# Performance work log

Measured on AMD Instinct MI355X. Metric: run time of the kernel, lower is better.

The kernel has to match this reference:

```python
import jax, jax.numpy as jnp
import numpy as np

EPS = 1e-5
GROUPS = 4


def gconv1x1(x, w, b, groups):
    # x: [B,C,H,W]; w: [Cout, Cin//groups]; grouped 1x1 conv
    B, C, H, W = x.shape
    Co = w.shape[0]
    xg = x.reshape(B, groups, C // groups, H, W)
    wg = w.reshape(groups, Co // groups, C // groups)
    y = jnp.einsum('bgchw,goc->bgohw', xg, wg).reshape(B, Co, H, W)
    if b is not None:
        y = y + b[None, :, None, None]
    return y


def setup_inputs() -> dict:
    key = jax.random.key(0)
    ks = jax.random.split(key, 9)
    B, C, H, W = 8, 64, 160, 160
    Cq = C // 8
    s = 0.1
    return {
        'x': jax.random.normal(ks[0], (B, C, H, W), jnp.float32),
        'wq': jax.random.normal(ks[1], (Cq, C // GROUPS), jnp.float32) * s,
        'bq': jax.random.normal(ks[2], (Cq,), jnp.float32) * s,
        'wk': jax.random.normal(ks[3], (Cq, C // GROUPS), jnp.float32) * s,
        'bk': jax.random.normal(ks[4], (Cq,), jnp.float32) * s,
        'wv': jax.random.normal(ks[5], (C, C // GROUPS), jnp.float32) * s,
        'bv': jax.random.normal(ks[6], (C,), jnp.float32) * s,
        'gamma': jax.random.normal(ks[7], (1,), jnp.float32) * s,
        'w1d': jax.random.normal(ks[8], (C, C // GROUPS), jnp.float32) * s,
        'bn_w': jnp.ones((C,), jnp.float32),
        'bn_b': jnp.zeros((C,), jnp.float32),
    }


def reference(x, wq, bq, wk, bk, wv, bv, gamma, w1d, bn_w, bn_b):
    B, C, H, W = x.shape
    q = gconv1x1(x, wq, bq, GROUPS)   # [B,Cq,H,W]
    k = gconv1x1(x, wk, bk, GROUPS)   # [B,Cq,H,W]
    v = gconv1x1(x, wv, bv, GROUPS)   # [B,C,H,W]

    # column (H) attention energies with -inf diagonal (self excluded on H path)
    energy_H = jnp.einsum('bchw,bcjw->bhwj', q, k)  # [B,H,W,H]
    diag = jnp.where(jnp.eye(H, dtype=bool), -jnp.inf, 0.0).astype(x.dtype)
    energy_H = energy_H + diag[:, None, :]
    # row (W) attention energies
    energy_W = jnp.einsum('bchw,bchj->bhwj', q, k)  # [B,H,W,W]

    att = jax.nn.softmax(jnp.concatenate([energy_H, energy_W], axis=3), axis=3)
    att_H = att[..., :H]           # [B,H,W,H]
    att_W = att[..., H:]           # [B,H,W,W]

    out_H = jnp.einsum('bcjw,bhwj->bchw', v, att_H)
    out_W = jnp.einsum('bchj,bhwj->bchw', v, att_W)
    out = gamma[0] * (out_H + out_W)               # [B,C,H,W]

    # kernel-size-1 grouped conv1d (dilation irrelevant for k=1), no bias
    L = H * W
    o = out.reshape(B, GROUPS, C // GROUPS, L)
    w1g = w1d.reshape(GROUPS, C // GROUPS, C // GROUPS)
    o = jnp.einsum('bgcl,goc->bgol', o, w1g).reshape(B, C, L)

    # BatchNorm1d (training mode: batch stats over (B, L), biased variance)
    mean = jnp.mean(o, axis=(0, 2), keepdims=True)
    var = jnp.mean((o - mean) ** 2, axis=(0, 2), keepdims=True)
    o = (o - mean) / jnp.sqrt(var + EPS) * bn_w[None, :, None] + bn_b[None, :, None]

    o = o.reshape(B, C, H, W)
    return jax.nn.relu(o + x)
```

## Files before the change

### kernel.cpp

```cpp
#include <hip/hip_runtime.h>
#include <math.h>

#define B_ 8
#define C_ 64
#define H_ 160
#define W_ 160
#define HW_ (H_*W_)

typedef _Float16 h2 __attribute__((ext_vector_type(2)));
typedef _Float16 h4 __attribute__((ext_vector_type(4)));
typedef _Float16 h8 __attribute__((ext_vector_type(8)));
typedef float f4v __attribute__((ext_vector_type(4)));
union H8u { h8 v; h2 h[4]; };

__device__ inline float fdot2(h2 a, h2 b, float c) {
    return __builtin_amdgcn_fdot2(a, b, c, false);
}

#define LOG2E 1.44269504088896f
#define ESH2  5.77078016355585f
#if __has_builtin(__builtin_amdgcn_exp2f)
#define EXP2F(x) __builtin_amdgcn_exp2f(x)
#else
#define EXP2F(x) exp2f(x)
#endif

static constexpr size_t N_PIX  = (size_t)B_*H_*W_;
static constexpr size_t N_FULL = (size_t)B_*H_*W_*C_;
static constexpr size_t OFF_OUTH  = 0;
static constexpr size_t OFF_VROW  = N_FULL/2;
static constexpr size_t OFF_QROW  = OFF_VROW + N_FULL/2;
static constexpr size_t OFF_KROW  = OFF_QROW + N_PIX*4;
static constexpr size_t OFF_MH    = OFF_KROW + N_PIX*4;
static constexpr size_t OFF_SH    = OFF_MH + N_PIX;
static constexpr size_t OFF_BNSUM = OFF_SH + N_PIX;
static constexpr size_t OFF_BNSQ  = OFF_BNSUM + 64;

__global__ __launch_bounds__(256,4) void qkv_kernel(
    const float* __restrict__ x,
    const float* __restrict__ wq, const float* __restrict__ bq,
    const float* __restrict__ wk, const float* __restrict__ bk,
    const float* __restrict__ wv, const float* __restrict__ bv,
    _Float16* __restrict__ qrow, _Float16* __restrict__ krow,
    _Float16* __restrict__ vrow)
{
    __shared__ __align__(16) _Float16 spool[10240];
    _Float16 (*xsh)[72] = (_Float16 (*)[72])spool;

    const int tid = threadIdx.x;
    const int w0 = blockIdx.x * 32;
    const int h0 = blockIdx.y * 4;
    const int b  = blockIdx.z;

    const float* xb = x + (size_t)b*C_*HW_;
    for (int i = tid; i < 2048; i += 256) {
        int w4 = i & 7;
        int c  = ((i >> 3) & 7) | (((i >> 6) & 7) << 3);
        int hh = i >> 9;
        float4 v = *(const float4*)(xb + (size_t)c*HW_ + (size_t)(h0+hh)*W_ + w0 + w4*4);
        int pix = hh*32 + w4*4;
        xsh[pix+0][c] = (_Float16)v.x; xsh[pix+1][c] = (_Float16)v.y;
        xsh[pix+2][c] = (_Float16)v.z; xsh[pix+3][c] = (_Float16)v.w;
    }
    __syncthreads();

    const int lane = tid & 63;
    const int wid  = tid >> 6;
    const int n16  = lane & 15;
    const int kg   = lane >> 4;
    const int pb   = wid * 32;

    h4 af[2][4];
    #pragma unroll
    for (int sub = 0; sub < 2; sub++)
        #pragma unroll
        for (int g = 0; g < 4; g++)
            af[sub][g] = *(const h4*)&xsh[pb + sub*16 + n16][g*16 + 4*kg];

    f4v vacc[2][4];
    #pragma unroll
    for (int g = 0; g < 4; g++) {
        float4 wf = *(const float4*)(wv + (g*16 + n16)*16 + 4*kg);
        h4 bf; bf[0]=(_Float16)wf.x; bf[1]=(_Float16)wf.y;
               bf[2]=(_Float16)wf.z; bf[3]=(_Float16)wf.w;
        const float bb = bv[g*16 + n16];
        #pragma unroll
        for (int sub = 0; sub < 2; sub++) {
            f4v c = {bb, bb, bb, bb};
            vacc[sub][g] = __builtin_amdgcn_mfma_f32_16x16x16f16(af[sub][g], bf, c, 0, 0, 0);
        }
    }
    f4v qkacc[2];
    {
        const int out = n16;
        const int gq  = (out & 7) >> 1;
        const float sc = (out < 8) ? LOG2E : 1.0f;
        const float* wp = ((out < 8) ? wq + out*16 : wk + (out-8)*16) + 4*kg;
        float4 wf = *(const float4*)wp;
        h4 bfq; bfq[0]=(_Float16)(wf.x*sc); bfq[1]=(_Float16)(wf.y*sc);
                bfq[2]=(_Float16)(wf.z*sc); bfq[3]=(_Float16)(wf.w*sc);
        h4 bz;  bz[0]=(_Float16)0; bz[1]=(_Float16)0; bz[2]=(_Float16)0; bz[3]=(_Float16)0;
        const float bb = ((out < 8) ? bq[out] : bk[out-8]) * sc;
        #pragma unroll
        for (int sub = 0; sub < 2; sub++) {
            f4v c = {bb, bb, bb, bb};
            #pragma unroll
            for (int g = 0; g < 4; g++) {
                h4 bg = (gq == g) ? bfq : bz;
                c = __builtin_amdgcn_mfma_f32_16x16x16f16(af[sub][g], bg, c, 0, 0, 0);
            }
            qkacc[sub] = c;
        }
    }
    __syncthreads();

    _Float16* vst = spool;
    _Float16* qks = spool + 8192;
    #pragma unroll
    for (int sub = 0; sub < 2; sub++) {
        #pragma unroll
        for (int r = 0; r < 4; r++) {
            int pix = pb + sub*16 + 4*kg + r;
            #pragma unroll
            for (int g = 0; g < 4; g++)
                vst[pix*64 + g*16 + n16] = (_Float16)vacc[sub][g][r];
            qks[pix*16 + n16] = (_Float16)qkacc[sub][r];
        }
    }
    __syncthreads();

    unsigned* vs32 = (unsigned*)spool;
    unsigned* qk32 = vs32 + 4096;
    unsigned* vrow32 = (unsigned*)vrow;
    for (int i = tid; i < 4096; i += 256) {
        int pix = i >> 5, cp = i & 31;
        size_t bp = ((size_t)b*H_ + h0 + (pix>>5))*W_ + w0 + (pix & 31);
        vrow32[bp*32 + cp] = vs32[i];
    }
    unsigned* qrow32 = (unsigned*)qrow;
    unsigned* krow32 = (unsigned*)krow;
    for (int i = tid; i < 1024; i += 256) {
        int pix = i >> 3, part = i & 7;
        size_t bp = ((size_t)b*H_ + h0 + (pix>>5))*W_ + w0 + (pix & 31);
        unsigned val = qk32[pix*8 + part];
        if (part < 4) qrow32[bp*4 + part]     = val;
        else          krow32[bp*4 + part - 4] = val;
    }
}

__global__ __launch_bounds__(256,4) void passA_kernel(
    const _Float16* __restrict__ qrow, const _Float16* __restrict__ krow,
    const _Float16* __restrict__ vrow,
    _Float16* __restrict__ outH, float* __restrict__ sH)
{
    __shared__ __align__(16) _Float16 pool[10240];
    __shared__ __align__(16) _Float16 q2h[160][8];
    __shared__ __align__(16) _Float16 k2h[160][8];
    __shared__ float psum2[2][2][32];

    _Float16* v2s = pool;

    const int tid = threadIdx.x;
    const int b = blockIdx.x / W_;
    const int w = blockIdx.x % W_;

    if (tid < 160) {
        size_t bp = ((size_t)b*H_ + tid)*W_ + w;
        *(int4*)&q2h[tid][0] = *(const int4*)(qrow + bp*8);
        *(int4*)&k2h[tid][0] = *(const int4*)(krow + bp*8);
    }
    {
        const unsigned* vr32 = (const unsigned*)vrow;
        const int cp = tid & 31, hp0 = tid >> 5;
        #pragma unroll 5
        for (int it = 0; it < 10; it++) {
            int hp = hp0 + 8*it;
            int kt = hp >> 4, dqv = (hp >> 2) & 3, jj = 2*(hp & 3);
            size_t bp0 = ((size_t)b*H_ + 2*hp)*W_ + w;
            unsigned u0 = vr32[bp0*32 + cp];
            unsigned u1 = vr32[(bp0 + W_)*32 + cp];
            unsigned e  = __builtin_amdgcn_perm(u1, u0, 0x05040100);
            unsigned o  = __builtin_amdgcn_perm(u1, u0, 0x07060302);
            int base = ((kt*4 + dqv)*64 + 2*cp)*8 + jj;
            *(unsigned*)&v2s[base]     = e;
            *(unsigned*)&v2s[base + 8] = o;
        }
    }
    __syncthreads();

    const int lane = tid & 63;
    const int wid  = tid >> 6;
    const int cM   = wid*16 + (lane & 15);
    const int m_   = lane & 15;
    const int dq   = lane >> 4;
    const int n16  = lane & 15;
    const int kg   = lane >> 4;
    const int qs   = wid & 1;
    const int jt0  = (wid >> 1)*5;

    h8 vfr[5];
    #pragma unroll
    for (int kt = 0; kt < 5; kt++)
        vfr[kt] = *(const h8*)&v2s[((kt*4 + dq)*64 + cM)*8];
    __syncthreads();

    for (int t = 0; t <= 5; t++) {
        if (t <= 4) {
            _Float16* Pts = pool + (t & 1)*5120;
            const int q32  = qs*16 + n16;
            const int qrw  = t*32 + q32;
            h4 qf = *(const h4*)&q2h[qrw][(kg & 1)*4];
            if (kg >= 2) { qf[0]=(_Float16)0; qf[1]=(_Float16)0; qf[2]=(_Float16)0; qf[3]=(_Float16)0; }
            float psloc = 0.f;
            #pragma unroll
            for (int jj = 0; jj < 5; jj++) {
                const int jt = jt0 + jj;
                h4 kf = *(const h4*)&k2h[jt*16 + n16][(kg & 1)*4];
                f4v d = {0.f,0.f,0.f,0.f};
                d = __builtin_amdgcn_mfma_f32_16x16x16f16(kf, qf, d, 0, 0, 0);
                const int grp = (jt >> 1)*4 + (jt & 1)*2 + (kg >> 1);
                h4 pk;
                #pragma unroll
                for (int r = 0; r < 4; r++) {
                    float p = EXP2F(d[r] - ESH2);
                    if (jt*16 + kg*4 + r == qrw) p = 0.f;
                    psloc += p;
                    pk[r] = (_Float16)p;
                }
                *(h4*)&Pts[(grp*32 + q32)*8 + (kg & 1)*4] = pk;
            }
            psloc += __shfl_xor(psloc, 16);
            psloc += __shfl_xor(psloc, 32);
            if (kg == 0) psum2[t & 1][wid >> 1][q32] = psloc;
        }
        if (t >= 1) {
            if (tid < 32) {
                sH[((size_t)b*W_ + w)*H_ + (t-1)*32 + tid] =
                    psum2[(t-1) & 1][0][tid] + psum2[(t-1) & 1][1][tid];
            }
            const _Float16* Pts = pool + ((t-1) & 1)*5120;
            f4v acc0 = {0.f,0.f,0.f,0.f}, acc1 = {0.f,0.f,0.f,0.f};
            #pragma unroll
            for (int kt = 0; kt < 5; kt++) {
                h8 a0  = *(const h8*)&Pts[((kt*4 + dq)*32 + m_)*8];
                h8 a1  = *(const h8*)&Pts[((kt*4 + dq)*32 + 16 + m_)*8];
                acc0 = __builtin_amdgcn_mfma_f32_16x16x32_f16(a0, vfr[kt], acc0, 0, 0, 0);
                acc1 = __builtin_amdgcn_mfma_f32_16x16x32_f16(a1, vfr[kt], acc1, 0, 0, 0);
            }
            #pragma unroll
            for (int r = 0; r < 4; r++) {
                int r0 = (t-1)*32 + dq*4 + r;
                outH[(((size_t)b*H_ + r0     )*W_ + w)*64 + cM] = (_Float16)acc0[r];
                outH[(((size_t)b*H_ + r0 + 16)*W_ + w)*64 + cM] = (_Float16)acc1[r];
            }
        }
        if (t <= 4) __syncthreads();
    }
}

__global__ __launch_bounds__(256,4) void passB_kernel(
    const _Float16* __restrict__ qrow, const _Float16* __restrict__ krow,
    const _Float16* vrow,
    const float* __restrict__ gamma, const float* __restrict__ w1d,
    const _Float16* __restrict__ outH, const float* __restrict__ sH,
    _Float16* o16, float* __restrict__ bnsum, float* __restrict__ bnsq)
{
    __shared__ __align__(16) _Float16 pool[10240];
    __shared__ __align__(16) _Float16 stageh[4*32*20];
    __shared__ __align__(16) _Float16 q2h[160][8];
    __shared__ __align__(16) _Float16 k2h[160][8];
    __shared__ float sHrow[160];
    __shared__ float psum2[2][2][32];

    _Float16* v2s = pool;

    const int tid = threadIdx.x;
    const int b = blockIdx.x / H_;
    const int h = blockIdx.x % H_;
    const float gam = gamma[0];

    const int lane = tid & 63;
    const int wid  = tid >> 6;
    const int cM   = wid*16 + (lane & 15);
    const int m_   = lane & 15;
    const int dq   = lane >> 4;
    const int n16  = lane & 15;
    const int kg   = lane >> 4;
    const int qs   = wid & 1;
    const int jt0  = (wid >> 1)*5;

    h4 w1f;
    {
        float4 wv4 = *(const float4*)(w1d + cM*16 + 4*dq);
        w1f[0] = (_Float16)wv4.x; w1f[1] = (_Float16)wv4.y;
        w1f[2] = (_Float16)wv4.z; w1f[3] = (_Float16)wv4.w;
    }

    const size_t rowbase = ((size_t)b*H_ + h)*W_;
    if (tid < 160) {
        size_t bp = rowbase + tid;
        *(int4*)&q2h[tid][0] = *(const int4*)(qrow + bp*8);
        *(int4*)&k2h[tid][0] = *(const int4*)(krow + bp*8);
        sHrow[tid] = sH[((size_t)b*W_ + tid)*H_ + h];
    }
    {
        const unsigned* vr32 = (const unsigned*)vrow;
        const int cp = tid & 31, wp0 = tid >> 5;
        #pragma unroll 5
        for (int it = 0; it < 10; it++) {
            int wp = wp0 + 8*it;
            int kt = wp >> 4, dqv = (wp >> 2) & 3, jj = 2*(wp & 3);
            size_t bp0 = rowbase + 2*wp;
            unsigned u0 = vr32[bp0*32 + cp];
            unsigned u1 = vr32[(bp0 + 1)*32 + cp];
            unsigned e  = __builtin_amdgcn_perm(u1, u0, 0x05040100);
            unsigned o  = __builtin_amdgcn_perm(u1, u0, 0x07060302);
            int base = ((kt*4 + dqv)*64 + 2*cp)*8 + jj;
            *(unsigned*)&v2s[base]     = e;
            *(unsigned*)&v2s[base + 8] = o;
        }
    }
    __syncthreads();

    h8 vfr[5];
    #pragma unroll
    for (int kt = 0; kt < 5; kt++)
        vfr[kt] = *(const h8*)&v2s[((kt*4 + dq)*64 + cM)*8];
    __syncthreads();

    float bnS = 0.f, bnS2 = 0.f;

    for (int t = 0; t <= 5; t++) {
        float oh0[4], oh1[4];
        if (t >= 1) {
            #pragma unroll
            for (int r = 0; r < 4; r++) {
                int rw0 = (t-1)*32 + dq*4 + r;
                oh0[r] = (float)outH[(rowbase + rw0     )*64 + cM];
                oh1[r] = (float)outH[(rowbase + rw0 + 16)*64 + cM];
            }
        }
        if (t <= 4) {
            _Float16* Pts = pool + (t & 1)*5120;
            const int q32 = qs*16 + n16;
            const int qrw = t*32 + q32;
            h4 qf = *(const h4*)&q2h[qrw][(kg & 1)*4];
            if (kg >= 2) { qf[0]=(_Float16)0; qf[1]=(_Float16)0; qf[2]=(_Float16)0; qf[3]=(_Float16)0; }
            float psloc = 0.f;
            #pragma unroll
            for (int jj = 0; jj < 5; jj++) {
                const int jt = jt0 + jj;
                h4 kf = *(const h4*)&k2h[jt*16 + n16][(kg & 1)*4];
                f4v d = {0.f,0.f,0.f,0.f};
                d = __builtin_amdgcn_mfma_f32_16x16x16f16(kf, qf, d, 0, 0, 0);
                const int grp = (jt >> 1)*4 + (jt & 1)*2 + (kg >> 1);
                h4 pk;
                #pragma unroll
                for (int r = 0; r < 4; r++) {
                    float p = EXP2F(d[r] - ESH2);
                    psloc += p;
                    pk[r] = (_Float16)p;
                }
                *(h4*)&Pts[(grp*32 + q32)*8 + (kg & 1)*4] = pk;
            }
            psloc += __shfl_xor(psloc, 16);
            psloc += __shfl_xor(psloc, 32);
            if (kg == 0) psum2[t & 1][wid >> 1][q32] = psloc;
        }
        if (t >= 1) {
            const int tp = t - 1;
            const _Float16* Pts = pool + (tp & 1)*5120;
            const int rl_ = lane & 31;
            float fval = gam / (sHrow[tp*32 + rl_]
                                + psum2[tp & 1][0][rl_] + psum2[tp & 1][1][rl_]);
            f4v acc0 = {0.f,0.f,0.f,0.f}, acc1 = {0.f,0.f,0.f,0.f};
            #pragma unroll
            for (int kt = 0; kt < 5; kt++) {
                h8 a0  = *(const h8*)&Pts[((kt*4 + dq)*32 + m_)*8];
                h8 a1  = *(const h8*)&Pts[((kt*4 + dq)*32 + 16 + m_)*8];
                acc0 = __builtin_amdgcn_mfma_f32_16x16x32_f16(a0, vfr[kt], acc0, 0, 0, 0);
                acc1 = __builtin_amdgcn_mfma_f32_16x16x32_f16(a1, vfr[kt], acc1, 0, 0, 0);
            }
            _Float16* st = &stageh[wid*640];
            #pragma unroll
            for (int r = 0; r < 4; r++) {
                int rl0 = dq*4 + r, rl1 = rl0 + 16;
                float f0 = __shfl(fval, rl0);
                float f1 = __shfl(fval, rl1);
                st[rl0*20 + m_] = (_Float16)((oh0[r] + acc0[r]) * f0);
                st[rl1*20 + m_] = (_Float16)((oh1[r] + acc1[r]) * f1);
            }
            h4 a0c = *(const h4*)&st[m_*20 + 4*dq];
            h4 a1c = *(const h4*)&st[(m_ + 16)*20 + 4*dq];
            f4v c0 = {0.f,0.f,0.f,0.f}, c1 = {0.f,0.f,0.f,0.f};
            c0 = __builtin_amdgcn_mfma_f32_16x16x16f16(a0c, w1f, c0, 0, 0, 0);
            c1 = __builtin_amdgcn_mfma_f32_16x16x16f16(a1c, w1f, c1, 0, 0, 0);
            #pragma unroll
            for (int r = 0; r < 4; r++) {
                int pr0 = dq*4 + r, pr1 = pr0 + 16;
                float o0 = c0[r], o1 = c1[r];
                o16[(rowbase + tp*32 + pr0)*64 + cM] = (_Float16)o0;
                o16[(rowbase + tp*32 + pr1)*64 + cM] = (_Float16)o1;
                bnS  += o0 + o1;
                bnS2 += o0*o0 + o1*o1;
            }
        }
        if (t <= 4) __syncthreads();
    }
    bnS  += __shfl_xor(bnS, 16);  bnS  += __shfl_xor(bnS, 32);
    bnS2 += __shfl_xor(bnS2, 16); bnS2 += __shfl_xor(bnS2, 32);
    if (dq == 0) {
        atomicAdd(&bnsum[cM], bnS);
        atomicAdd(&bnsq[cM],  bnS2);
    }
}

__global__ __launch_bounds__(256) void final_kernel(
    const float* __restrict__ x, const _Float16* __restrict__ o16,
    const float* __restrict__ bnsum, const float* __restrict__ bnsq,
    const float* __restrict__ bn_w, const float* __restrict__ bn_b,
    float* __restrict__ out)
{
    __shared__ _Float16 olds[160*66];
    __shared__ float sc[64], sh[64];
    const int tid = threadIdx.x;
    const int b = blockIdx.x / H_, h = blockIdx.x % H_;
    if (tid < 64) {
        const float cnt = (float)(B_*H_*W_);
        float mean = bnsum[tid] / cnt;
        float var  = bnsq[tid] / cnt - mean*mean;
        float istd = rsqrtf(var + 1e-5f);
        float scl  = bn_w[tid] * istd;
        sc[tid] = scl;
        sh[tid] = bn_b[tid] - mean*scl;
    }
    const unsigned* op = (const unsigned*)(o16 + ((size_t)b*H_ + h)*W_*64);
    unsigned* ol32 = (unsigned*)olds;
    for (int i = tid; i < 5120; i += 256) {
        int w = i >> 5, c2 = i & 31;
        ol32[w*33 + c2] = op[i];
    }
    __syncthreads();
    const float* xr = x   + (size_t)b*C_*HW_ + (size_t)h*W_;
    float*       ob = out + (size_t)b*C_*HW_ + (size_t)h*W_;
    for (int i = tid; i < 64*160; i += 256) {
        int c = i / 160, w = i - c*160;
        float v = (float)olds[w*66 + c] * sc[c] + sh[c] + xr[(size_t)c*HW_ + w];
        ob[(size_t)c*HW_ + w] = fmaxf(v, 0.f);
    }
}

extern "C" void kernel_launch(void* const* d_in, const int* in_sizes, int n_in,
                              void* d_out, int out_size, void* d_ws, size_t ws_size,
                              hipStream_t stream)
{
    (void)in_sizes; (void)n_in; (void)out_size; (void)ws_size;
    const float* x     = (const float*)d_in[0];
    const float* wq    = (const float*)d_in[1];
    const float* bq    = (const float*)d_in[2];
    const float* wk    = (const float*)d_in[3];
    const float* bk    = (const float*)d_in[4];
    const float* wv    = (const float*)d_in[5];
    const float* bv    = (const float*)d_in[6];
    const float* gamma = (const float*)d_in[7];
    const float* w1d   = (const float*)d_in[8];
    const float* bn_w  = (const float*)d_in[9];
    const float* bn_b  = (const float*)d_in[10];

    float* ws = (float*)d_ws;
    _Float16* outH16 = (_Float16*)(ws + OFF_OUTH);
    _Float16* vrow   = (_Float16*)(ws + OFF_VROW);
    _Float16* qrow   = (_Float16*)(ws + OFF_QROW);
    _Float16* krow   = (_Float16*)(ws + OFF_KROW);
    float* sH    = ws + OFF_SH;
    float* bnsum = ws + OFF_BNSUM;
    float* bnsq  = ws + OFF_BNSQ;
    _Float16* o16 = vrow;

    (void)hipMemsetAsync(bnsum, 0, 128*sizeof(float), stream);

    dim3 qgrid(W_/32, H_/4, B_);
    qkv_kernel<<<qgrid, 256, 0, stream>>>(x, wq, bq, wk, bk, wv, bv, qrow, krow, vrow);
    passA_kernel<<<B_*W_, 256, 0, stream>>>(qrow, krow, vrow, outH16, sH);
    passB_kernel<<<B_*H_, 256, 0, stream>>>(qrow, krow, vrow, gamma, w1d,
                                            outH16, sH, o16, bnsum, bnsq);
    final_kernel<<<B_*H_, 256, 0, stream>>>(x, o16, bnsum, bnsq, bn_w, bn_b, (float*)d_out);
}
```

Measured before the change: 206.7 us.

## Split attention passes across query tiles into separate blocks, write output in place

Pass A and pass B now launch five blocks per column or row, one per 32-query tile, where before one block looped over all five tiles with double-buffered P. This adds parallelism and drops the per-tile loop and its barriers. In exchange, each block reloads the full V column or row and the K vectors, so V staging traffic goes up fivefold. Pass B also writes its conv output back into the outH buffer in place instead of a separate o16 buffer, and BN atomics now fire once per block, five times as often.

```diff
diff --git a/kernel.cpp b/kernel.cpp
--- a/kernel.cpp
+++ b/kernel.cpp
@@ -154,20 +154,27 @@
     _Float16* __restrict__ outH, float* __restrict__ sH)
 {
     __shared__ __align__(16) _Float16 pool[10240];
-    __shared__ __align__(16) _Float16 q2h[160][8];
+    __shared__ __align__(16) _Float16 q2h[32][8];
     __shared__ __align__(16) _Float16 k2h[160][8];
-    __shared__ float psum2[2][2][32];
+    __shared__ float psum2[2][32];
 
     _Float16* v2s = pool;
+    _Float16* Pts = pool;
 
     const int tid = threadIdx.x;
-    const int b = blockIdx.x / W_;
-    const int w = blockIdx.x % W_;
+    const int bx  = blockIdx.x;
+    const int t   = bx % 5;
+    const int col = bx / 5;
+    const int b = col / W_;
+    const int w = col % W_;
 
     if (tid < 160) {
         size_t bp = ((size_t)b*H_ + tid)*W_ + w;
-        *(int4*)&q2h[tid][0] = *(const int4*)(qrow + bp*8);
         *(int4*)&k2h[tid][0] = *(const int4*)(krow + bp*8);
+        if (tid < 32) {
+            size_t bq = ((size_t)b*H_ + t*32 + tid)*W_ + w;
+            *(int4*)&q2h[tid][0] = *(const int4*)(qrow + bq*8);
+        }
     }
     {
         const unsigned* vr32 = (const unsigned*)vrow;
@@ -204,79 +211,78 @@
         vfr[kt] = *(const h8*)&v2s[((kt*4 + dq)*64 + cM)*8];
     __syncthreads();
 
-    for (int t = 0; t <= 5; t++) {
-        if (t <= 4) {
-            _Float16* Pts = pool + (t & 1)*5120;
-            const int q32  = qs*16 + n16;
-            const int qrw  = t*32 + q32;
-            h4 qf = *(const h4*)&q2h[qrw][(kg & 1)*4];
-            if (kg >= 2) { qf[0]=(_Float16)0; qf[1]=(_Float16)0; qf[2]=(_Float16)0; qf[3]=(_Float16)0; }
-            float psloc = 0.f;
-            #pragma unroll
-            for (int jj = 0; jj < 5; jj++) {
-                const int jt = jt0 + jj;
-                h4 kf = *(const h4*)&k2h[jt*16 + n16][(kg & 1)*4];
-                f4v d = {0.f,0.f,0.f,0.f};
-                d = __builtin_amdgcn_mfma_f32_16x16x16f16(kf, qf, d, 0, 0, 0);
-                const int grp = (jt >> 1)*4 + (jt & 1)*2 + (kg >> 1);
-                h4 pk;
-                #pragma unroll
-                for (int r = 0; r < 4; r++) {
-                    float p = EXP2F(d[r] - ESH2);
-                    if (jt*16 + kg*4 + r == qrw) p = 0.f;
-                    psloc += p;
-                    pk[r] = (_Float16)p;
-                }
-                *(h4*)&Pts[(grp*32 + q32)*8 + (kg & 1)*4] = pk;
-            }
-            psloc += __shfl_xor(psloc, 16);
-            psloc += __shfl_xor(psloc, 32);
-            if (kg == 0) psum2[t & 1][wid >> 1][q32] = psloc;
-        }
-        if (t >= 1) {
-            if (tid < 32) {
-                sH[((size_t)b*W_ + w)*H_ + (t-1)*32 + tid] =
-                    psum2[(t-1) & 1][0][tid] + psum2[(t-1) & 1][1][tid];
-            }
-            const _Float16* Pts = pool + ((t-1) & 1)*5120;
-            f4v acc0 = {0.f,0.f,0.f,0.f}, acc1 = {0.f,0.f,0.f,0.f};
-            #pragma unroll
-            for (int kt = 0; kt < 5; kt++) {
-                h8 a0  = *(const h8*)&Pts[((kt*4 + dq)*32 + m_)*8];
-                h8 a1  = *(const h8*)&Pts[((kt*4 + dq)*32 + 16 + m_)*8];
-                acc0 = __builtin_amdgcn_mfma_f32_16x16x32_f16(a0, vfr[kt], acc0, 0, 0, 0);
-                acc1 = __builtin_amdgcn_mfma_f32_16x16x32_f16(a1, vfr[kt], acc1, 0, 0, 0);
-            }
+    {
+        const int q32  = qs*16 + n16;
+        const int qrw  = t*32 + q32;
+        h4 qf = *(const h4*)&q2h[q32][(kg & 1)*4];
+        if (kg >= 2) { qf[0]=(_Float16)0; qf[1]=(_Float16)0; qf[2]=(_Float16)0; qf[3]=(_Float16)0; }
+        float psloc = 0.f;
+        #pragma unroll
+        for (int jj = 0; jj < 5; jj++) {
+            const int jt = jt0 + jj;
+            h4 kf = *(const h4*)&k2h[jt*16 + n16][(kg & 1)*4];
+            f4v d = {0.f,0.f,0.f,0.f};
+            d = __builtin_amdgcn_mfma_f32_16x16x16f16(kf, qf, d, 0, 0, 0);
+            const int grp = (jt >> 1)*4 + (jt & 1)*2 + (kg >> 1);
+            h4 pk;
             #pragma unroll
             for (int r = 0; r < 4; r++) {
-                int r0 = (t-1)*32 + dq*4 + r;
-                outH[(((size_t)b*H_ + r0     )*W_ + w)*64 + cM] = (_Float16)acc0[r];
-                outH[(((size_t)b*H_ + r0 + 16)*W_ + w)*64 + cM] = (_Float16)acc1[r];
+                float p = EXP2F(d[r] - ESH2);
+                if (jt*16 + kg*4 + r == qrw) p = 0.f;
+                psloc += p;
+                pk[r] = (_Float16)p;
             }
-        }
-        if (t <= 4) __syncthreads();
+            *(h4*)&Pts[(grp*32 + q32)*8 + (kg & 1)*4] = pk;
+        }
+        psloc += __shfl_xor(psloc, 16);
+        psloc += __shfl_xor(psloc, 32);
+        if (kg == 0) psum2[wid >> 1][q32] = psloc;
+    }
+    __syncthreads();
+
+    if (tid < 32)
+        sH[((size_t)b*W_ + w)*H_ + t*32 + tid] = psum2[0][tid] + psum2[1][tid];
+
+    f4v acc0 = {0.f,0.f,0.f,0.f}, acc1 = {0.f,0.f,0.f,0.f};
+    #pragma unroll
+    for (int kt = 0; kt < 5; kt++) {
+        h8 a0  = *(const h8*)&Pts[((kt*4 + dq)*32 + m_)*8];
+        h8 a1  = *(const h8*)&Pts[((kt*4 + dq)*32 + 16 + m_)*8];
+        acc0 = __builtin_amdgcn_mfma_f32_16x16x32_f16(a0, vfr[kt], acc0, 0, 0, 0);
+        acc1 = __builtin_amdgcn_mfma_f32_16x16x32_f16(a1, vfr[kt], acc1, 0, 0, 0);
+    }
+    #pragma unroll
+    for (int r = 0; r < 4; r++) {
+        int r0 = t*32 + dq*4 + r;
+        outH[(((size_t)b*H_ + r0     )*W_ + w)*64 + cM] = (_Float16)acc0[r];
+        outH[(((size_t)b*H_ + r0 + 16)*W_ + w)*64 + cM] = (_Float16)acc1[r];
     }
 }
 
 __global__ __launch_bounds__(256,4) void passB_kernel(
     const _Float16* __restrict__ qrow, const _Float16* __restrict__ krow,
-    const _Float16* vrow,
+    const _Float16* __restrict__ vrow,
     const float* __restrict__ gamma, const float* __restrict__ w1d,
-    const _Float16* __restrict__ outH, const float* __restrict__ sH,
-    _Float16* o16, float* __restrict__ bnsum, float* __restrict__ bnsq)
+    _Float16* outHio,
+    const float* __restrict__ sH,
+    float* __restrict__ bnsum, float* __restrict__ bnsq)
 {
     __shared__ __align__(16) _Float16 pool[10240];
-    __shared__ __align__(16) _Float16 stageh[4*32*20];
-    __shared__ __align__(16) _Float16 q2h[160][8];
+    __shared__ __align__(16) _Float16 q2h[32][8];
     __shared__ __align__(16) _Float16 k2h[160][8];
-    __shared__ float sHrow[160];
-    __shared__ float psum2[2][2][32];
+    __shared__ float sHrow[32];
+    __shared__ float psum2[2][32];
 
     _Float16* v2s = pool;
+    _Float16* Pts = pool;
+    _Float16* stageh = pool + 5120;
 
     const int tid = threadIdx.x;
-    const int b = blockIdx.x / H_;
-    const int h = blockIdx.x % H_;
+    const int bx  = blockIdx.x;
+    const int t   = bx % 5;
+    const int row = bx / 5;
+    const int b = row / H_;
+    const int h = row % H_;
     const float gam = gamma[0];
 
     const int lane = tid & 63;
@@ -299,9 +305,12 @@
     const size_t rowbase = ((size_t)b*H_ + h)*W_;
     if (tid < 160) {
         size_t bp = rowbase + tid;
-        *(int4*)&q2h[tid][0] = *(const int4*)(qrow + bp*8);
         *(int4*)&k2h[tid][0] = *(const int4*)(krow + bp*8);
-        sHrow[tid] = sH[((size_t)b*W_ + tid)*H_ + h];
+        if (tid < 32) {
+            size_t bq = rowbase + t*32 + tid;
+            *(int4*)&q2h[tid][0] = *(const int4*)(qrow + bq*8);
+            sHrow[tid] = sH[((size_t)b*W_ + t*32 + tid)*H_ + h];
+        }
     }
     {
         const unsigned* vr32 = (const unsigned*)vrow;
@@ -326,86 +335,77 @@
     #pragma unroll
     for (int kt = 0; kt < 5; kt++)
         vfr[kt] = *(const h8*)&v2s[((kt*4 + dq)*64 + cM)*8];
-    __syncthreads();
-
-    float bnS = 0.f, bnS2 = 0.f;
-
-    for (int t = 0; t <= 5; t++) {
-        float oh0[4], oh1[4];
-        if (t >= 1) {
+
+    float oh0[4], oh1[4];
+    #pragma unroll
+    for (int r = 0; r < 4; r++) {
+        int rw0 = t*32 + dq*4 + r;
+        oh0[r] = (float)outHio[(rowbase + rw0     )*64 + cM];
+        oh1[r] = (float)outHio[(rowbase + rw0 + 16)*64 + cM];
+    }
+    __syncthreads();
+
+    {
+        const int q32 = qs*16 + n16;
+        h4 qf = *(const h4*)&q2h[q32][(kg & 1)*4];
+        if (kg >= 2) { qf[0]=(_Float16)0; qf[1]=(_Float16)0; qf[2]=(_Float16)0; qf[3]=(_Float16)0; }
+        float psloc = 0.f;
+        #pragma unroll
+        for (int jj = 0; jj < 5; jj++) {
+            const int jt = jt0 + jj;
+            h4 kf = *(const h4*)&k2h[jt*16 + n16][(kg & 1)*4];
+            f4v d = {0.f,0.f,0.f,0.f};
+            d = __builtin_amdgcn_mfma_f32_16x16x16f16(kf, qf, d, 0, 0, 0);
+            const int grp = (jt >> 1)*4 + (jt & 1)*2 + (kg >> 1);
+            h4 pk;
             #pragma unroll
             for (int r = 0; r < 4; r++) {
-                int rw0 = (t-1)*32 + dq*4 + r;
-                oh0[r] = (float)outH[(rowbase + rw0     )*64 + cM];
-                oh1[r] = (float)outH[(rowbase + rw0 + 16)*64 + cM];
+                float p = EXP2F(d[r] - ESH2);
+                psloc += p;
+                pk[r] = (_Float16)p;
             }
-        }
-        if (t <= 4) {
-            _Float16* Pts = pool + (t & 1)*5120;
-            const int q32 = qs*16 + n16;
-            const int qrw = t*32 + q32;
-            h4 qf = *(const h4*)&q2h[qrw][(kg & 1)*4];
-            if (kg >= 2) { qf[0]=(_Float16)0; qf[1]=(_Float16)0; qf[2]=(_Float16)0; qf[3]=(_Float16)0; }
-            float psloc = 0.f;
-            #pragma unroll
-            for (int jj = 0; jj < 5; jj++) {
-                const int jt = jt0 + jj;
-                h4 kf = *(const h4*)&k2h[jt*16 + n16][(kg & 1)*4];
-                f4v d = {0.f,0.f,0.f,0.f};
-                d = __builtin_amdgcn_mfma_f32_16x16x16f16(kf, qf, d, 0, 0, 0);
-                const int grp = (jt >> 1)*4 + (jt & 1)*2 + (kg >> 1);
-                h4 pk;
-                #pragma unroll
-                for (int r = 0; r < 4; r++) {
-                    float p = EXP2F(d[r] - ESH2);
-                    psloc += p;
-                    pk[r] = (_Float16)p;
-                }
-                *(h4*)&Pts[(grp*32 + q32)*8 + (kg & 1)*4] = pk;
-            }
-            psloc += __shfl_xor(psloc, 16);
-            psloc += __shfl_xor(psloc, 32);
-            if (kg == 0) psum2[t & 1][wid >> 1][q32] = psloc;
-        }
-        if (t >= 1) {
-            const int tp = t - 1;
-            const _Float16* Pts = pool + (tp & 1)*5120;
-            const int rl_ = lane & 31;
-            float fval = gam / (sHrow[tp*32 + rl_]
-                                + psum2[tp & 1][0][rl_] + psum2[tp & 1][1][rl_]);
-            f4v acc0 = {0.f,0.f,0.f,0.f}, acc1 = {0.f,0.f,0.f,0.f};
-            #pragma unroll
-            for (int kt = 0; kt < 5; kt++) {
-                h8 a0  = *(const h8*)&Pts[((kt*4 + dq)*32 + m_)*8];
-                h8 a1  = *(const h8*)&Pts[((kt*4 + dq)*32 + 16 + m_)*8];
-                acc0 = __builtin_amdgcn_mfma_f32_16x16x32_f16(a0, vfr[kt], acc0, 0, 0, 0);
-                acc1 = __builtin_amdgcn_mfma_f32_16x16x32_f16(a1, vfr[kt], acc1, 0, 0, 0);
-            }
-            _Float16* st = &stageh[wid*640];
-            #pragma unroll
-            for (int r = 0; r < 4; r++) {
-                int rl0 = dq*4 + r, rl1 = rl0 + 16;
-                float f0 = __shfl(fval, rl0);
-                float f1 = __shfl(fval, rl1);
-                st[rl0*20 + m_] = (_Float16)((oh0[r] + acc0[r]) * f0);
-                st[rl1*20 + m_] = (_Float16)((oh1[r] + acc1[r]) * f1);
-            }
-            h4 a0c = *(const h4*)&st[m_*20 + 4*dq];
-            h4 a1c = *(const h4*)&st[(m_ + 16)*20 + 4*dq];
-            f4v c0 = {0.f,0.f,0.f,0.f}, c1 = {0.f,0.f,0.f,0.f};
-            c0 = __builtin_amdgcn_mfma_f32_16x16x16f16(a0c, w1f, c0, 0, 0, 0);
-            c1 = __builtin_amdgcn_mfma_f32_16x16x16f16(a1c, w1f, c1, 0, 0, 0);
-            #pragma unroll
-            for (int r = 0; r < 4; r++) {
-                int pr0 = dq*4 + r, pr1 = pr0 + 16;
-                float o0 = c0[r], o1 = c1[r];
-                o16[(rowbase + tp*32 + pr0)*64 + cM] = (_Float16)o0;
-                o16[(rowbase + tp*32 + pr1)*64 + cM] = (_Float16)o1;
-                bnS  += o0 + o1;
-                bnS2 += o0*o0 + o1*o1;
-            }
-        }
-        if (t <= 4) __syncthreads();
+            *(h4*)&Pts[(grp*32 + q32)*8 + (kg & 1)*4] = pk;
+        }
+        psloc += __shfl_xor(psloc, 16);
+        psloc += __shfl_xor(psloc, 32);
+        if (kg == 0) psum2[wid >> 1][q32] = psloc;
+    }
+    __syncthreads();
+
+    const int rl_ = lane & 31;
+    float fval = gam / (sHrow[rl_] + psum2[0][rl_] + psum2[1][rl_]);
+
+    f4v acc0 = {0.f,0.f,0.f,0.f}, acc1 = {0.f,0.f,0.f,0.f};
+    #pragma unroll
+    for (int kt = 0; kt < 5; kt++) {
+        h8 a0  = *(const h8*)&Pts[((kt*4 + dq)*32 + m_)*8];
+        h8 a1  = *(const h8*)&Pts[((kt*4 + dq)*32 + 16 + m_)*8];
+        acc0 = __builtin_amdgcn_mfma_f32_16x16x32_f16(a0, vfr[kt], acc0, 0, 0, 0);
+        acc1 = __builtin_amdgcn_mfma_f32_16x16x32_f16(a1, vfr[kt], acc1, 0, 0, 0);
+    }
+    _Float16* st = &stageh[wid*640];
+    #pragma unroll
+    for (int r = 0; r < 4; r++) {
+        int rl0 = dq*4 + r, rl1 = rl0 + 16;
+        float f0 = __shfl(fval, rl0);
+        float f1 = __shfl(fval, rl1);
+        st[rl0*20 + m_] = (_Float16)((oh0[r] + acc0[r]) * f0);
+        st[rl1*20 + m_] = (_Float16)((oh1[r] + acc1[r]) * f1);
+    }
+    h4 a0c = *(const h4*)&st[m_*20 + 4*dq];
+    h4 a1c = *(const h4*)&st[(m_ + 16)*20 + 4*dq];
+    f4v c0 = {0.f,0.f,0.f,0.f}, c1 = {0.f,0.f,0.f,0.f};
+    c0 = __builtin_amdgcn_mfma_f32_16x16x16f16(a0c, w1f, c0, 0, 0, 0);
+    c1 = __builtin_amdgcn_mfma_f32_16x16x16f16(a1c, w1f, c1, 0, 0, 0);
+    float bnS = 0.f, bnS2 = 0.f;
+    #pragma unroll
+    for (int r = 0; r < 4; r++) {
+        int pr0 = dq*4 + r, pr1 = pr0 + 16;
+        float o0 = c0[r], o1 = c1[r];
+        outHio[(rowbase + t*32 + pr0)*64 + cM] = (_Float16)o0;
+        outHio[(rowbase + t*32 + pr1)*64 + cM] = (_Float16)o1;
+        bnS  += o0 + o1;
+        bnS2 += o0*o0 + o1*o1;
     }
     bnS  += __shfl_xor(bnS, 16);  bnS  += __shfl_xor(bnS, 32);
     bnS2 += __shfl_xor(bnS2, 16); bnS2 += __shfl_xor(bnS2, 32);
@@ -475,14 +475,13 @@
     float* sH    = ws + OFF_SH;
     float* bnsum = ws + OFF_BNSUM;
     float* bnsq  = ws + OFF_BNSQ;
-    _Float16* o16 = vrow;
 
     (void)hipMemsetAsync(bnsum, 0, 128*sizeof(float), stream);
 
     dim3 qgrid(W_/32, H_/4, B_);
     qkv_kernel<<<qgrid, 256, 0, stream>>>(x, wq, bq, wk, bk, wv, bv, qrow, krow, vrow);
-    passA_kernel<<<B_*W_, 256, 0, stream>>>(qrow, krow, vrow, outH16, sH);
-    passB_kernel<<<B_*H_, 256, 0, stream>>>(qrow, krow, vrow, gamma, w1d,
-                                            outH16, sH, o16, bnsum, bnsq);
-    final_kernel<<<B_*H_, 256, 0, stream>>>(x, o16, bnsum, bnsq, bn_w, bn_b, (float*)d_out);
-}
+    passA_kernel<<<B_*W_*5, 256, 0, stream>>>(qrow, krow, vrow, outH16, sH);
+    passB_kernel<<<B_*H_*5, 256, 0, stream>>>(qrow, krow, vrow, gamma, w1d,
+                                              outH16, sH, bnsum, bnsq);
+    final_kernel<<<B_*H_, 256, 0, stream>>>(x, outH16, bnsum, bnsq, bn_w, bn_b, (float*)d_out);
+}
```

New measurement: 332.6 us. 1.61x slower.
